# Kernel optimization log

Measured on AMD Instinct MI355X. Metric: run time of the kernel, lower is better.

## Reference

```python
import jax, jax.numpy as jnp
import numpy as np

EMBED = 1024
HEADS = 16
HEAD_DIM = EMBED // HEADS


def setup_inputs() -> dict:
    key = jax.random.key(0)
    ks = jax.random.split(key, 8)
    N, S, E = 4, 2048, EMBED
    s = 1.0 / np.sqrt(E)
    return {
        "values": jax.random.normal(ks[0], (N, S, E), jnp.float32),
        "keys": jax.random.normal(ks[1], (N, S, E), jnp.float32),
        "queries": jax.random.normal(ks[2], (N, S, E), jnp.float32),
        # nn.Linear weights stored as (out_features, in_features)
        "Wv": jax.random.normal(ks[3], (E, E), jnp.float32) * s,
        "Wk": jax.random.normal(ks[4], (E, E), jnp.float32) * s,
        "Wq": jax.random.normal(ks[5], (E, E), jnp.float32) * s,
        "Wo": jax.random.normal(ks[6], (E, E), jnp.float32) * s,
        "bo": jax.random.normal(ks[7], (E,), jnp.float32) * s,
    }


def reference(values, keys, queries, Wv, Wk, Wq, Wo, bo):
    N = queries.shape[0]
    H, D, E = HEADS, HEAD_DIM, EMBED
    # projections (torch Linear: x @ W.T), reshape to [N, S, H, D]
    v = (values @ Wv.T).reshape(N, -1, H, D)
    k = (keys @ Wk.T).reshape(N, -1, H, D)
    q = (queries @ Wq.T).reshape(N, -1, H, D)
    energy = jnp.einsum("nqhd,nkhd->nhqk", q, k)
    # NOTE: original scales by sqrt(embed_size), not sqrt(head_dim)
    attn = jax.nn.softmax(energy / jnp.sqrt(jnp.float32(E)), axis=3)
    out = jnp.einsum("nhql,nlhd->nqhd", attn, v).reshape(N, -1, H * D)
    return out @ Wo.T + bo
```

## Files before the change

kernel.cpp:

```cpp
#include <hip/hip_runtime.h>

typedef __bf16  bf16x8 __attribute__((ext_vector_type(8)));
typedef __bf16  bf16x4 __attribute__((ext_vector_type(4)));
typedef short   s16x4  __attribute__((ext_vector_type(4)));
typedef float   f32x4  __attribute__((ext_vector_type(4)));

__device__ __forceinline__ unsigned short f2bf(float f) {
    union { float f; unsigned int u; } v; v.f = f;
    unsigned int u = v.u;
    unsigned int r = (u + 0x7fffu + ((u >> 16) & 1u)) >> 16;
    return (unsigned short)r;
}

__device__ __forceinline__ unsigned int pkbf(float lo, float hi) {
    union { float f; unsigned int u; } a, b; a.f = lo; b.f = hi;
    return __builtin_amdgcn_perm(b.u + 0x8000u, a.u + 0x8000u, 0x07060302u);
}

__device__ __forceinline__ float fexp2(float x) {
#if __has_builtin(__builtin_amdgcn_exp2f)
    return __builtin_amdgcn_exp2f(x);
#else
    float r; asm("v_exp_f32 %0, %1\n\ts_nop 1" : "=v"(r) : "v"(x)); return r;
#endif
}

__device__ __forceinline__ void gld_lds16(const unsigned short* g, unsigned short* l) {
    auto gp = (const __attribute__((address_space(1))) unsigned int*)(const void*)g;
    auto lp = (__attribute__((address_space(3))) unsigned int*)(unsigned int)(unsigned long long)(void*)l;
    __builtin_amdgcn_global_load_lds(gp, lp, 16, 0, 0);
}

__device__ __forceinline__ f32x4 mfma16(bf16x4 a, bf16x4 b, f32x4 c) {
#if __has_builtin(__builtin_amdgcn_mfma_f32_16x16x16_bf16)
    return __builtin_amdgcn_mfma_f32_16x16x16_bf16(a, b, c, 0, 0, 0);
#elif __has_builtin(__builtin_amdgcn_mfma_f32_16x16x16bf16_1k)
    union U { bf16x4 h; s16x4 s; } ua, ub; ua.h = a; ub.h = b;
    return __builtin_amdgcn_mfma_f32_16x16x16bf16_1k(ua.s, ub.s, c, 0, 0, 0);
#else
    asm("v_mfma_f32_16x16x16_bf16 %0, %1, %2, %0" : "+v"(c) : "v"(a), "v"(b));
    return c;
#endif
}

__global__ void cast4_kernel(const float* __restrict__ a, const float* __restrict__ b,
                             const float* __restrict__ c, const float* __restrict__ d,
                             unsigned short* __restrict__ dst) {
    int sel = blockIdx.x >> 10;
    int off4 = (blockIdx.x & 1023) * 256 + threadIdx.x;
    const float* src = sel == 0 ? a : sel == 1 ? b : sel == 2 ? c : d;
    float4 f = ((const float4*)src)[off4];
    uint2 pk; pk.x = pkbf(f.x, f.y); pk.y = pkbf(f.z, f.w);
    ((uint2*)(dst + (size_t)sel * 1048576))[off4] = pk;
}

__global__ __launch_bounds__(256, 3)
void gemm_qkv(const float* __restrict__ V32, const float* __restrict__ K32,
              const float* __restrict__ Q32, const unsigned short* __restrict__ W,
              unsigned short* __restrict__ Vtb, unsigned short* __restrict__ Kb,
              unsigned short* __restrict__ Qb, float qscale)
{
    constexpr int K = 1024;
    __shared__ unsigned short As[2][4096];
    __shared__ unsigned short Bs[2][4096];

    const int z = blockIdx.z;
    const float* A32 = z == 0 ? V32 : z == 1 ? K32 : Q32;
    const unsigned short* Bt = W + (size_t)z * 1048576;
    unsigned short* dst = z == 0 ? Vtb : z == 1 ? Kb : Qb;
    const float a_scale = z == 2 ? qscale : 1.f;

    const int t    = threadIdx.x;
    const int lane = t & 63;
    const int w    = t >> 6;
    const int q    = lane >> 4;
    const int ln   = lane & 15;
    const int wr   = w >> 1, wc = w & 1;
    const int m0   = blockIdx.x * 128;
    const int n0   = blockIdx.y * 128;
    const int srow = lane >> 2;
    const int scol = (lane & 3) * 8;

    f32x4 acc[4][4];
    const f32x4 zz = {0.f, 0.f, 0.f, 0.f};
#pragma unroll
    for (int i = 0; i < 4; ++i)
#pragma unroll
        for (int j = 0; j < 4; ++j) acc[i][j] = zz;

    auto loadA = [&](int k0, float4* fa) {
#pragma unroll
        for (int c = 0; c < 2; ++c) {
            int u = w * 2 + c;
            const float* src = A32 + (size_t)(m0 + u * 16 + srow) * K + k0 + scol;
            fa[c * 2]     = *(const float4*)src;
            fa[c * 2 + 1] = *(const float4*)(src + 4);
        }
    };
    auto writeA = [&](const float4* fa, int p) {
#pragma unroll
        for (int c = 0; c < 2; ++c) {
            int u = w * 2 + c;
            uint4 pk;
            pk.x = pkbf(fa[c * 2].x,     fa[c * 2].y);
            pk.y = pkbf(fa[c * 2].z,     fa[c * 2].w);
            pk.z = pkbf(fa[c * 2 + 1].x, fa[c * 2 + 1].y);
            pk.w = pkbf(fa[c * 2 + 1].z, fa[c * 2 + 1].w);
            *(uint4*)&As[p][u * 512 + lane * 8] = pk;
        }
    };
    auto stageB = [&](int k0, int p) {
#pragma unroll
        for (int c = 0; c < 2; ++c) {
            int u = w * 2 + c;
            gld_lds16(Bt + (size_t)(n0 + u * 16 + srow) * K + k0 + scol, &Bs[p][u * 512]);
        }
    };

    float4 fa[4];
    loadA(0, fa);
    stageB(0, 0);
    writeA(fa, 0);
    for (int j = 0; j < 32; ++j) {
        __syncthreads();
        if (j < 31) { loadA((j + 1) * 32, fa); stageB((j + 1) * 32, (j + 1) & 1); }
        const int p = j & 1;
        bf16x8 af[4], bfr[4];
#pragma unroll
        for (int i = 0; i < 4; ++i)
            af[i] = *(const bf16x8*)&As[p][(wr * 64 + i * 16 + ln) * 32 + q * 8];
#pragma unroll
        for (int jj = 0; jj < 4; ++jj)
            bfr[jj] = *(const bf16x8*)&Bs[p][(wc * 64 + jj * 16 + ln) * 32 + q * 8];
#pragma unroll
        for (int i = 0; i < 4; ++i)
#pragma unroll
            for (int jj = 0; jj < 4; ++jj)
                acc[i][jj] = __builtin_amdgcn_mfma_f32_16x16x32_bf16(af[i], bfr[jj], acc[i][jj], 0, 0, 0);
        if (j < 31) writeA(fa, (j + 1) & 1);
    }

#pragma unroll
    for (int i = 0; i < 4; ++i) {
#pragma unroll
        for (int jj = 0; jj < 4; ++jj) {
            f32x4 c = acc[i][jj];
            int mb = m0 + wr * 64 + i * 16 + q * 4;
            int nn = n0 + wc * 64 + jj * 16 + ln;
            if (z == 0) {
                int b = mb >> 11, s = mb & 2047, h = nn >> 6, d = nn & 63;
                uint2 pk;
                pk.x = pkbf(c[0], c[1]);
                pk.y = pkbf(c[2], c[3]);
                size_t idx = (((size_t)(b * 16 + h) * 64) + d) * 2048 + s;
                *(uint2*)&dst[idx] = pk;
            } else {
#pragma unroll
                for (int r = 0; r < 4; ++r) {
                    int m = mb + r;
                    float val = c[r] * a_scale;
                    int b = m >> 11, s = m & 2047, h = nn >> 6, d = nn & 63;
                    size_t idx = (((size_t)(b * 16 + h) * 2048) + s) * 64 + d;
                    dst[idx] = f2bf(val);
                }
            }
        }
    }
}

template <int MODE>
__global__ __launch_bounds__(256, 3)
void gemm_bt(const unsigned short* __restrict__ A, const unsigned short* __restrict__ Bt,
             void* __restrict__ dst, const float* __restrict__ bias, float a_scale)
{
    constexpr int K = 1024;
    __shared__ unsigned short As[2][4096];
    __shared__ unsigned short Bs[2][4096];

    const int t    = threadIdx.x;
    const int lane = t & 63;
    const int w    = t >> 6;
    const int q    = lane >> 4;
    const int ln   = lane & 15;
    const int wr   = w >> 1, wc = w & 1;
    const int m0   = blockIdx.x * 128;
    const int n0   = blockIdx.y * 128;
    const int srow = lane >> 2;
    const int scol = (lane & 3) * 8;

    f32x4 acc[4][4];
    const f32x4 zz = {0.f, 0.f, 0.f, 0.f};
#pragma unroll
    for (int i = 0; i < 4; ++i)
#pragma unroll
        for (int j = 0; j < 4; ++j) acc[i][j] = zz;

    auto stage = [&](int k0, int p) {
#pragma unroll
        for (int c = 0; c < 2; ++c) {
            int u = w * 2 + c;
            gld_lds16(A  + (size_t)(m0 + u * 16 + srow) * K + k0 + scol, &As[p][u * 512]);
            gld_lds16(Bt + (size_t)(n0 + u * 16 + srow) * K + k0 + scol, &Bs[p][u * 512]);
        }
    };

    stage(0, 0);
    for (int j = 0; j < 32; ++j) {
        __syncthreads();
        if (j < 31) stage((j + 1) * 32, (j + 1) & 1);
        const int p = j & 1;
        bf16x8 af[4], bfr[4];
#pragma unroll
        for (int i = 0; i < 4; ++i)
            af[i] = *(const bf16x8*)&As[p][(wr * 64 + i * 16 + ln) * 32 + q * 8];
#pragma unroll
        for (int jj = 0; jj < 4; ++jj)
            bfr[jj] = *(const bf16x8*)&Bs[p][(wc * 64 + jj * 16 + ln) * 32 + q * 8];
#pragma unroll
        for (int i = 0; i < 4; ++i)
#pragma unroll
            for (int jj = 0; jj < 4; ++jj)
                acc[i][jj] = __builtin_amdgcn_mfma_f32_16x16x32_bf16(af[i], bfr[jj], acc[i][jj], 0, 0, 0);
    }

#pragma unroll
    for (int i = 0; i < 4; ++i) {
#pragma unroll
        for (int j = 0; j < 4; ++j) {
            f32x4 c = acc[i][j];
            int mb = m0 + wr * 64 + i * 16 + q * 4;
            int nn = n0 + wc * 64 + j * 16 + ln;
#pragma unroll
            for (int r = 0; r < 4; ++r) {
                int m = mb + r;
                float val = c[r] * a_scale;
                ((float*)dst)[(size_t)m * 1024 + nn] = val + bias[nn];
            }
        }
    }
}

__global__ __launch_bounds__(256, 4)
void attn_kernel(const unsigned short* __restrict__ Q, const unsigned short* __restrict__ Kg,
                 const unsigned short* __restrict__ Vt, unsigned short* __restrict__ Og)
{
    __shared__ __align__(16) unsigned short Ks[2][4096];
    __shared__ __align__(16) unsigned short Vs[2][4096];

    const int t    = threadIdx.x;
    const int lane = t & 63;
    const int w    = t >> 6;
    const int q    = lane >> 4;
    const int ln   = lane & 15;
    const int xs   = (ln >> 1) & 3;
    const int head = blockIdx.x;
    const int qt   = blockIdx.y;

    const unsigned short* Qh  = Q  + (size_t)head * 2048 * 64;
    const unsigned short* Kh  = Kg + (size_t)head * 2048 * 64;
    const unsigned short* Vth = Vt + (size_t)head * 64 * 2048;

    const int srow = lane >> 2;
    const int ssw  = ((lane & 3) ^ ((lane >> 3) & 3)) * 8;

    bf16x8 qf[2][2];
    const int rowb = qt * 128 + w * 32;
#pragma unroll
    for (int ti = 0; ti < 2; ++ti)
#pragma unroll
        for (int kc = 0; kc < 2; ++kc)
            qf[ti][kc] = *(const bf16x8*)&Qh[(size_t)(rowb + ti * 16 + ln) * 64 + kc * 32 + q * 8];

    const f32x4 zz = {0.f, 0.f, 0.f, 0.f};
    f32x4 oa[2][4];
#pragma unroll
    for (int ti = 0; ti < 2; ++ti)
#pragma unroll
        for (int dt = 0; dt < 4; ++dt) oa[ti][dt] = zz;
    float l_s[2] = {0.f, 0.f};

    auto stage = [&](int j, int p) {
#pragma unroll
        for (int c = 0; c < 2; ++c) {
            int u = w * 2 + c;
            int kc = u >> 2, rg = u & 3;
            gld_lds16(Kh + (size_t)(j * 64 + rg * 16 + srow) * 64 + kc * 32 + ssw,
                      &Ks[p][kc * 2048 + rg * 512]);
            gld_lds16(Vth + (size_t)(rg * 16 + srow) * 2048 + j * 64 + kc * 32 + ssw,
                      &Vs[p][kc * 2048 + rg * 512]);
        }
    };

    stage(0, 0);
    for (int j = 0; j < 32; ++j) {
        __syncthreads();
        if (j < 31) stage(j + 1, (j + 1) & 1);
        const int p = j & 1;

        bf16x4 pb[4][2];
        float rs0 = 0.f, rs1 = 0.f;
#pragma unroll
        for (int kt = 0; kt < 4; ++kt) {
            f32x4 s0 = zz, s1 = zz;
#pragma unroll
            for (int kc = 0; kc < 2; ++kc) {
                bf16x8 ka = *(const bf16x8*)&Ks[p][kc * 2048 + (kt * 16 + ln) * 32 + ((q ^ xs) * 8)];
                s0 = __builtin_amdgcn_mfma_f32_16x16x32_bf16(ka, qf[0][kc], s0, 0, 0, 0);
                s1 = __builtin_amdgcn_mfma_f32_16x16x32_bf16(ka, qf[1][kc], s1, 0, 0, 0);
            }
            {
                float a0 = fexp2(s0[0]), a1 = fexp2(s0[1]), a2 = fexp2(s0[2]), a3 = fexp2(s0[3]);
                rs0 += (a0 + a1) + (a2 + a3);
                f32x4 pe = {a0, a1, a2, a3};
                pb[kt][0] = __builtin_convertvector(pe, bf16x4);
            }
            {
                float b0 = fexp2(s1[0]), b1 = fexp2(s1[1]), b2 = fexp2(s1[2]), b3 = fexp2(s1[3]);
                rs1 += (b0 + b1) + (b2 + b3);
                f32x4 pe = {b0, b1, b2, b3};
                pb[kt][1] = __builtin_convertvector(pe, bf16x4);
            }
        }
        l_s[0] += rs0;
        l_s[1] += rs1;

#pragma unroll
        for (int kt = 0; kt < 4; ++kt) {
            const int kc = kt >> 1;
            const int so = ((((kt & 1) * 2 + (q >> 1)) ^ xs) * 8) + (q & 1) * 4;
            bf16x4 va[4];
#pragma unroll
            for (int dt = 0; dt < 4; ++dt)
                va[dt] = *(const bf16x4*)&Vs[p][kc * 2048 + (dt * 16 + ln) * 32 + so];
#pragma unroll
            for (int dt = 0; dt < 4; ++dt) {
                oa[0][dt] = mfma16(va[dt], pb[kt][0], oa[0][dt]);
                oa[1][dt] = mfma16(va[dt], pb[kt][1], oa[1][dt]);
            }
        }
    }

    l_s[0] += __shfl_xor(l_s[0], 16); l_s[0] += __shfl_xor(l_s[0], 32);
    l_s[1] += __shfl_xor(l_s[1], 16); l_s[1] += __shfl_xor(l_s[1], 32);

    const int n = head >> 4;
    const int hbase = (head & 15) * 64;
#pragma unroll
    for (int ti = 0; ti < 2; ++ti) {
        float inv = 1.f / l_s[ti];
        int sr = qt * 128 + w * 32 + ti * 16 + ln;
        size_t base = ((size_t)n * 2048 + sr) * 1024 + hbase;
#pragma unroll
        for (int dt = 0; dt < 4; ++dt) {
            uint2 pk;
            pk.x = pkbf(oa[ti][dt][0] * inv, oa[ti][dt][1] * inv);
            pk.y = pkbf(oa[ti][dt][2] * inv, oa[ti][dt][3] * inv);
            *(uint2*)&Og[base + dt * 16 + q * 4] = pk;
        }
    }
}

extern "C" void kernel_launch(void* const* d_in, const int* in_sizes, int n_in,
                              void* d_out, int out_size, void* d_ws, size_t ws_size,
                              hipStream_t stream)
{
    (void)in_sizes; (void)n_in; (void)out_size; (void)ws_size;
    const float* values  = (const float*)d_in[0];
    const float* keys    = (const float*)d_in[1];
    const float* queries = (const float*)d_in[2];
    const float* Wv = (const float*)d_in[3];
    const float* Wk = (const float*)d_in[4];
    const float* Wq = (const float*)d_in[5];
    const float* Wo = (const float*)d_in[6];
    const float* bo = (const float*)d_in[7];
    float* out = (float*)d_out;

    unsigned short* ws   = (unsigned short*)d_ws;
    unsigned short* Wo_b = ws + 3145728;
    unsigned short* Ob   = ws + 4194304;
    unsigned short* Qb   = ws + 12582912;
    unsigned short* Kb   = Qb + 8388608;
    unsigned short* Vtb  = Kb + 8388608;

    const float qscale = 1.4426950408889634f / 32.f;
    dim3 b(256);

    cast4_kernel<<<4096, b, 0, stream>>>(Wv, Wk, Wq, Wo, ws);
    gemm_qkv<<<dim3(64, 8, 3), b, 0, stream>>>(values, keys, queries, ws, Vtb, Kb, Qb, qscale);
    attn_kernel<<<dim3(64, 16), b, 0, stream>>>(Qb, Kb, Vtb, Ob);
    gemm_bt<2><<<dim3(64, 8), b, 0, stream>>>(Ob, Wo_b, out, bo, 1.f);
}
```

Measured before the change: 343.1 us.

## Load QKV GEMM operands directly from global into registers, dropping LDS staging

The QKV projection GEMM no longer stages A and B tiles through shared memory with barriers. Each wave loads its own fp32 A rows and bf16 weight rows straight into MFMA fragment registers, converting A to bf16 in registers, with register double-buffering across K steps. This removes LDS writes, reads and __syncthreads. In exchange, A and B tiles are no longer shared between waves, so global and L2 traffic rises about twofold, and the extra register buffers may lower occupancy.

```diff
diff --git a/kernel.cpp b/kernel.cpp
--- a/kernel.cpp
+++ b/kernel.cpp
@@ -15,6 +15,13 @@
 __device__ __forceinline__ unsigned int pkbf(float lo, float hi) {
     union { float f; unsigned int u; } a, b; a.f = lo; b.f = hi;
     return __builtin_amdgcn_perm(b.u + 0x8000u, a.u + 0x8000u, 0x07060302u);
+}
+
+__device__ __forceinline__ bf16x8 pack8(float4 lo, float4 hi) {
+    union { unsigned int u[4]; bf16x8 v; } r;
+    r.u[0] = pkbf(lo.x, lo.y); r.u[1] = pkbf(lo.z, lo.w);
+    r.u[2] = pkbf(hi.x, hi.y); r.u[3] = pkbf(hi.z, hi.w);
+    return r.v;
 }
 
 __device__ __forceinline__ float fexp2(float x) {
@@ -60,10 +67,6 @@
               unsigned short* __restrict__ Vtb, unsigned short* __restrict__ Kb,
               unsigned short* __restrict__ Qb, float qscale)
 {
-    constexpr int K = 1024;
-    __shared__ unsigned short As[2][4096];
-    __shared__ unsigned short Bs[2][4096];
-
     const int z = blockIdx.z;
     const float* A32 = z == 0 ? V32 : z == 1 ? K32 : Q32;
     const unsigned short* Bt = W + (size_t)z * 1048576;
@@ -78,8 +81,15 @@
     const int wr   = w >> 1, wc = w & 1;
     const int m0   = blockIdx.x * 128;
     const int n0   = blockIdx.y * 128;
-    const int srow = lane >> 2;
-    const int scol = (lane & 3) * 8;
+
+    const float* Ar0 = A32 + (size_t)(m0 + wr * 64 +  0 + ln) * 1024 + q * 8;
+    const float* Ar1 = A32 + (size_t)(m0 + wr * 64 + 16 + ln) * 1024 + q * 8;
+    const float* Ar2 = A32 + (size_t)(m0 + wr * 64 + 32 + ln) * 1024 + q * 8;
+    const float* Ar3 = A32 + (size_t)(m0 + wr * 64 + 48 + ln) * 1024 + q * 8;
+    const unsigned short* Br0 = Bt + (size_t)(n0 + wc * 64 +  0 + ln) * 1024 + q * 8;
+    const unsigned short* Br1 = Bt + (size_t)(n0 + wc * 64 + 16 + ln) * 1024 + q * 8;
+    const unsigned short* Br2 = Bt + (size_t)(n0 + wc * 64 + 32 + ln) * 1024 + q * 8;
+    const unsigned short* Br3 = Bt + (size_t)(n0 + wc * 64 + 48 + ln) * 1024 + q * 8;
 
     f32x4 acc[4][4];
     const f32x4 zz = {0.f, 0.f, 0.f, 0.f};
@@ -88,56 +98,58 @@
 #pragma unroll
         for (int j = 0; j < 4; ++j) acc[i][j] = zz;
 
-    auto loadA = [&](int k0, float4* fa) {
-#pragma unroll
-        for (int c = 0; c < 2; ++c) {
-            int u = w * 2 + c;
-            const float* src = A32 + (size_t)(m0 + u * 16 + srow) * K + k0 + scol;
-            fa[c * 2]     = *(const float4*)src;
-            fa[c * 2 + 1] = *(const float4*)(src + 4);
-        }
+    auto LOADA = [&](float4* la, int j) {
+        la[0] = *(const float4*)(Ar0 + j * 32); la[1] = *(const float4*)(Ar0 + j * 32 + 4);
+        la[2] = *(const float4*)(Ar1 + j * 32); la[3] = *(const float4*)(Ar1 + j * 32 + 4);
+        la[4] = *(const float4*)(Ar2 + j * 32); la[5] = *(const float4*)(Ar2 + j * 32 + 4);
+        la[6] = *(const float4*)(Ar3 + j * 32); la[7] = *(const float4*)(Ar3 + j * 32 + 4);
     };
-    auto writeA = [&](const float4* fa, int p) {
-#pragma unroll
-        for (int c = 0; c < 2; ++c) {
-            int u = w * 2 + c;
-            uint4 pk;
-            pk.x = pkbf(fa[c * 2].x,     fa[c * 2].y);
-            pk.y = pkbf(fa[c * 2].z,     fa[c * 2].w);
-            pk.z = pkbf(fa[c * 2 + 1].x, fa[c * 2 + 1].y);
-            pk.w = pkbf(fa[c * 2 + 1].z, fa[c * 2 + 1].w);
-            *(uint4*)&As[p][u * 512 + lane * 8] = pk;
-        }
+    auto LOADB = [&](bf16x8* bf, int j) {
+        bf[0] = *(const bf16x8*)(Br0 + j * 32);
+        bf[1] = *(const bf16x8*)(Br1 + j * 32);
+        bf[2] = *(const bf16x8*)(Br2 + j * 32);
+        bf[3] = *(const bf16x8*)(Br3 + j * 32);
     };
-    auto stageB = [&](int k0, int p) {
-#pragma unroll
-        for (int c = 0; c < 2; ++c) {
-            int u = w * 2 + c;
-            gld_lds16(Bt + (size_t)(n0 + u * 16 + srow) * K + k0 + scol, &Bs[p][u * 512]);
-        }
+    auto STEP = [&](const float4* la, const bf16x8* bf) {
+        bf16x8 af[4];
+#pragma unroll
+        for (int i = 0; i < 4; ++i) af[i] = pack8(la[2 * i], la[2 * i + 1]);
+#pragma unroll
+        for (int i = 0; i < 4; ++i)
+#pragma unroll
+            for (int jj = 0; jj < 4; ++jj)
+                acc[i][jj] = __builtin_amdgcn_mfma_f32_16x16x32_bf16(af[i], bf[jj], acc[i][jj], 0, 0, 0);
     };
 
-    float4 fa[4];
-    loadA(0, fa);
-    stageB(0, 0);
-    writeA(fa, 0);
-    for (int j = 0; j < 32; ++j) {
-        __syncthreads();
-        if (j < 31) { loadA((j + 1) * 32, fa); stageB((j + 1) * 32, (j + 1) & 1); }
-        const int p = j & 1;
-        bf16x8 af[4], bfr[4];
-#pragma unroll
-        for (int i = 0; i < 4; ++i)
-            af[i] = *(const bf16x8*)&As[p][(wr * 64 + i * 16 + ln) * 32 + q * 8];
-#pragma unroll
-        for (int jj = 0; jj < 4; ++jj)
-            bfr[jj] = *(const bf16x8*)&Bs[p][(wc * 64 + jj * 16 + ln) * 32 + q * 8];
-#pragma unroll
-        for (int i = 0; i < 4; ++i)
-#pragma unroll
-            for (int jj = 0; jj < 4; ++jj)
-                acc[i][jj] = __builtin_amdgcn_mfma_f32_16x16x32_bf16(af[i], bfr[jj], acc[i][jj], 0, 0, 0);
-        if (j < 31) writeA(fa, (j + 1) & 1);
+    float4 la[8];
+    bf16x8 bfA[4], bfB[4];
+    LOADA(la, 0);
+    LOADB(bfA, 0);
+#pragma unroll
+    for (int j = 0; j < 32; j += 2) {
+        {
+            bf16x8 af[4];
+#pragma unroll
+            for (int i = 0; i < 4; ++i) af[i] = pack8(la[2 * i], la[2 * i + 1]);
+            LOADB(bfB, j + 1);
+            LOADA(la, j + 1);
+#pragma unroll
+            for (int i = 0; i < 4; ++i)
+#pragma unroll
+                for (int jj = 0; jj < 4; ++jj)
+                    acc[i][jj] = __builtin_amdgcn_mfma_f32_16x16x32_bf16(af[i], bfA[jj], acc[i][jj], 0, 0, 0);
+        }
+        {
+            bf16x8 af[4];
+#pragma unroll
+            for (int i = 0; i < 4; ++i) af[i] = pack8(la[2 * i], la[2 * i + 1]);
+            if (j + 2 < 32) { LOADB(bfA, j + 2); LOADA(la, j + 2); }
+#pragma unroll
+            for (int i = 0; i < 4; ++i)
+#pragma unroll
+                for (int jj = 0; jj < 4; ++jj)
+                    acc[i][jj] = __builtin_amdgcn_mfma_f32_16x16x32_bf16(af[i], bfB[jj], acc[i][jj], 0, 0, 0);
+        }
     }
 
 #pragma unroll
```

After: 511.0 us. 1.49x slower.
